# Performance work log

Hardware: AMD Instinct MI355X
Metric: run time of the kernel (lower is better)

The kernel has to match this reference:

```python
import jax, jax.numpy as jnp
import numpy as np

DEPTH, B, H, E = 4, 4096, 1024, 1024  # embedDim == h so all layers stack


def setup_inputs() -> dict:
    key = jax.random.key(0)
    k1, k2, k3, k4 = jax.random.split(key, 4)
    x = jax.random.normal(k1, (B, E), dtype=jnp.float32)
    s_h = jax.random.normal(k2, (DEPTH, B, H), dtype=jnp.float32)
    s_c = jax.random.normal(k3, (DEPTH, B, H), dtype=jnp.float32)
    # Linear(embedDim + h, 4h) per layer; stored as [in, out] (transposed torch layout)
    W = jax.random.normal(k4, (DEPTH, E + H, 4 * H), dtype=jnp.float32) * 0.02
    b = jnp.zeros((DEPTH, 4 * H), dtype=jnp.float32)
    return {"x": x, "s_h": s_h, "s_c": s_c, "W": W, "b": b}


def _lstm_layer(out, layer_params):
    hh, c, Wl, bl = layer_params
    xh = jnp.concatenate([out, hh], axis=1)          # [B, E+H]
    z = xh @ Wl + bl                                  # [B, 4H]
    i, f, o, g = jnp.split(z, 4, axis=1)              # torch.split(Wx, h, 1) order: i,f,o,g
    i = jax.nn.sigmoid(i)
    f = jax.nn.sigmoid(f)
    o = jax.nn.sigmoid(o)
    g = jnp.tanh(g)
    # trainable=False -> no dropout on g
    c_new = c * f + g * i
    h_new = jnp.tanh(c_new) * o
    return h_new, (h_new, c_new)


def reference(x, s_h, s_c, W, b):
    # scan over depth: layer l consumes previous layer's output as its input
    out, (h_new, c_new) = jax.lax.scan(_lstm_layer, x, (s_h, s_c, W, b))
    return out, h_new, c_new
```

## Files before the change

kernel.cpp:

```cpp
#include <hip/hip_runtime.h>
#include <hip/hip_bf16.h>
#include <stdint.h>

#define DEPTH 4
#define Bb 4096
#define Hh 1024
#define Ee 1024
#define Kd 2048
#define Ng 4096

typedef __attribute__((ext_vector_type(8))) short short8;
typedef __attribute__((ext_vector_type(4))) float floatx4;
typedef __attribute__((ext_vector_type(4))) float f32x4;

__device__ __forceinline__ float fast_sigmoid(float x) {
  return 1.0f / (1.0f + __expf(-x));
}
__device__ __forceinline__ float fast_tanh(float x) {
  float t = __expf(-2.0f * fabsf(x));
  return copysignf((1.0f - t) / (1.0f + t), x);
}

__device__ __forceinline__ void gload_lds16(const void* g, void* l) {
  __builtin_amdgcn_global_load_lds(
      (const __attribute__((address_space(1))) void*)(uintptr_t)g,
      (__attribute__((address_space(3))) void*)(uint32_t)(uintptr_t)l,
      16, 0, 0);
}

__global__ __launch_bounds__(256) void transpose_w_kernel(
    const float* __restrict__ W, __hip_bfloat16* __restrict__ Wt) {
  __shared__ float tile[32][33];
  const int l = blockIdx.z;
  const int n0 = blockIdx.x * 32;
  const int k0 = blockIdx.y * 32;
  const float* Wl = W + (size_t)l * Kd * Ng;
  __hip_bfloat16* Wtl = Wt + (size_t)l * Ng * Kd;
  const int tx = threadIdx.x, ty = threadIdx.y;
#pragma unroll
  for (int q = 0; q < 4; q++) {
    tile[ty + q * 8][tx] = Wl[(size_t)(k0 + ty + q * 8) * Ng + n0 + tx];
  }
  __syncthreads();
#pragma unroll
  for (int q = 0; q < 4; q++) {
    Wtl[(size_t)(n0 + ty + q * 8) * Kd + k0 + tx] =
        __float2bfloat16(tile[tx][ty + q * 8]);
  }
}

__global__ __launch_bounds__(256) void prefill_xh_kernel(
    const float* __restrict__ x, const float* __restrict__ s_h,
    __hip_bfloat16* __restrict__ xh) {
  const int idx = blockIdx.x * blockDim.x + threadIdx.x;
  const int XN = Bb * Ee / 4;
  const int TOTAL = XN + DEPTH * Bb * Hh / 4;
  if (idx >= TOTAL) return;
  const float* srcp;
  __hip_bfloat16* dst;
  if (idx < XN) {
    const int b = idx >> 8;
    const int j4 = idx & 255;
    srcp = x + (size_t)idx * 4;
    dst = xh + (size_t)b * Kd + j4 * 4;
  } else {
    const int e4 = idx - XN;
    const int l = e4 >> 20;
    const int r = e4 & 0xFFFFF;
    const int b = r >> 8;
    const int j4 = r & 255;
    srcp = s_h + (size_t)e4 * 4;
    dst = xh + (size_t)l * Bb * Kd + (size_t)b * Kd + Ee + j4 * 4;
  }
  f32x4 v = *(const f32x4*)srcp;
  union {
    __hip_bfloat16 h[4];
    unsigned long long u;
  } p;
  p.h[0] = __float2bfloat16(v.x);
  p.h[1] = __float2bfloat16(v.y);
  p.h[2] = __float2bfloat16(v.z);
  p.h[3] = __float2bfloat16(v.w);
  *(unsigned long long*)dst = p.u;
}

__global__ __launch_bounds__(256, 2) void lstm_layer_kernel(
    const __hip_bfloat16* __restrict__ A, const __hip_bfloat16* __restrict__ Wt,
    const float* __restrict__ bias, const float* __restrict__ c_in,
    float* __restrict__ out_h, float* __restrict__ out_c,
    float* __restrict__ out_final, __hip_bfloat16* __restrict__ xh_next) {
  __shared__ __attribute__((aligned(16))) __hip_bfloat16 As[128][32];
  __shared__ __attribute__((aligned(16))) __hip_bfloat16 Bs[128][32];

  const int tid = threadIdx.x;
  const int lane = tid & 63;
  const int wave = tid >> 6;
  const int wm = wave >> 1;
  const int wn = wave & 1;
  const int m0 = blockIdx.y * 128;
  const int j0 = blockIdx.x * 32;

  const int seg = (tid & 3) * 8;
  const int ra0 = tid >> 2;
  const int ra1 = (tid + 256) >> 2;
  const __hip_bfloat16* a_src0 = A + (size_t)(m0 + ra0) * Kd + seg;
  const __hip_bfloat16* a_src1 = A + (size_t)(m0 + ra1) * Kd + seg;
  const int nb0 = (ra0 >> 5) * Hh + j0 + (ra0 & 31);
  const int nb1 = (ra1 >> 5) * Hh + j0 + (ra1 & 31);
  const __hip_bfloat16* b_src0 = Wt + (size_t)nb0 * Kd + seg;
  const __hip_bfloat16* b_src1 = Wt + (size_t)nb1 * Kd + seg;
  __hip_bfloat16* a_dst0 = &As[0][0] + tid * 8;
  __hip_bfloat16* a_dst1 = &As[0][0] + (tid + 256) * 8;
  __hip_bfloat16* b_dst0 = &Bs[0][0] + tid * 8;
  __hip_bfloat16* b_dst1 = &Bs[0][0] + (tid + 256) * 8;

  floatx4 acc[4][4];
#pragma unroll
  for (int mi = 0; mi < 4; mi++)
#pragma unroll
    for (int g = 0; g < 4; g++) acc[mi][g] = floatx4{0.f, 0.f, 0.f, 0.f};

  const int lm = lane & 15;
  const int qk = lane >> 4;

  for (int kt = 0; kt < Kd / 32; kt++) {
    const int koff = kt * 32;
    __syncthreads();
    gload_lds16(a_src0 + koff, a_dst0);
    gload_lds16(a_src1 + koff, a_dst1);
    gload_lds16(b_src0 + koff, b_dst0);
    gload_lds16(b_src1 + koff, b_dst1);
    __syncthreads();

    short8 afrag[4], bfrag[4];
#pragma unroll
    for (int mi = 0; mi < 4; mi++)
      afrag[mi] = *(const short8*)&As[wm * 64 + mi * 16 + lm][qk * 8];
#pragma unroll
    for (int g = 0; g < 4; g++)
      bfrag[g] = *(const short8*)&Bs[g * 32 + wn * 16 + lm][qk * 8];
#pragma unroll
    for (int mi = 0; mi < 4; mi++)
#pragma unroll
      for (int g = 0; g < 4; g++)
        acc[mi][g] = __builtin_amdgcn_mfma_f32_16x16x32_bf16(
            afrag[mi], bfrag[g], acc[mi][g], 0, 0, 0);
  }

  const int j = j0 + wn * 16 + lm;
  const float bi = bias[j];
  const float bf = bias[Hh + j];
  const float bo = bias[2 * Hh + j];
  const float bg = bias[3 * Hh + j];
#pragma unroll
  for (int mi = 0; mi < 4; mi++) {
    const int row0 = m0 + wm * 64 + mi * 16 + qk * 4;
#pragma unroll
    for (int r = 0; r < 4; r++) {
      const int row = row0 + r;
      const float zi = acc[mi][0][r] + bi;
      const float zf = acc[mi][1][r] + bf;
      const float zo = acc[mi][2][r] + bo;
      const float zg = acc[mi][3][r] + bg;
      const float ig = fast_sigmoid(zi);
      const float fg = fast_sigmoid(zf);
      const float og = fast_sigmoid(zo);
      const float gg = fast_tanh(zg);
      const float c = c_in[(size_t)row * Hh + j];
      const float cn = fmaf(c, fg, gg * ig);
      const float hn = fast_tanh(cn) * og;
      out_h[(size_t)row * Hh + j] = hn;
      out_c[(size_t)row * Hh + j] = cn;
      if (xh_next) xh_next[(size_t)row * Kd + j] = __float2bfloat16(hn);
      if (out_final) out_final[(size_t)row * Hh + j] = hn;
    }
  }
}

extern "C" void kernel_launch(void* const* d_in, const int* in_sizes, int n_in,
                              void* d_out, int out_size, void* d_ws,
                              size_t ws_size, hipStream_t stream) {
  const float* x = (const float*)d_in[0];
  const float* s_h = (const float*)d_in[1];
  const float* s_c = (const float*)d_in[2];
  const float* W = (const float*)d_in[3];
  const float* bias = (const float*)d_in[4];
  float* out = (float*)d_out;

  __hip_bfloat16* Wt = (__hip_bfloat16*)d_ws;
  __hip_bfloat16* xh =
      (__hip_bfloat16*)((char*)d_ws + (size_t)DEPTH * Ng * Kd * 2);

  transpose_w_kernel<<<dim3(Ng / 32, Kd / 32, DEPTH), dim3(32, 8), 0, stream>>>(
      W, Wt);
  prefill_xh_kernel<<<(Bb * Ee / 4 + DEPTH * Bb * Hh / 4) / 256, 256, 0,
                      stream>>>(x, s_h, xh);

  float* out_h = out + (size_t)Bb * Ee;
  float* out_c = out_h + (size_t)DEPTH * Bb * Hh;
  for (int l = 0; l < DEPTH; l++) {
    lstm_layer_kernel<<<dim3(Hh / 32, Bb / 128), 256, 0, stream>>>(
        xh + (size_t)l * Bb * Kd, Wt + (size_t)l * Ng * Kd,
        bias + (size_t)l * Ng, s_c + (size_t)l * Bb * Hh,
        out_h + (size_t)l * Bb * Hh, out_c + (size_t)l * Bb * Hh,
        (l == DEPTH - 1) ? out : nullptr,
        (l < DEPTH - 1) ? xh + (size_t)(l + 1) * Bb * Kd : nullptr);
  }
}
```

Measured before the change: 757.7 us.

## Swizzle GEMM LDS tiles and vectorize weight transpose kernel

The GEMM's LDS tiles get an XOR swizzle on the 16-byte chunk index, applied to the global source offsets used by global_load_lds and to the fragment read offsets, to cut LDS bank conflicts on the MFMA fragment loads. Fragment offsets are precomputed once, outside the k-loop. The weight transpose kernel is rewritten to use float4 global loads into a wider padded tile and 16-byte bf16 stores of 8 k-values per thread, to improve memory coalescing. The swizzle must stay consistent between the load and read paths, and the new transpose tile has a different shared-memory bank pattern.

Measured after the change: 753.9 us. No clear change (-0.5%).

```diff
diff --git a/kernel.cpp b/kernel.cpp
--- a/kernel.cpp
+++ b/kernel.cpp
@@ -30,23 +30,30 @@
 
 __global__ __launch_bounds__(256) void transpose_w_kernel(
     const float* __restrict__ W, __hip_bfloat16* __restrict__ Wt) {
-  __shared__ float tile[32][33];
+  __shared__ __attribute__((aligned(16))) float tile[32][68];
   const int l = blockIdx.z;
-  const int n0 = blockIdx.x * 32;
-  const int k0 = blockIdx.y * 32;
-  const float* Wl = W + (size_t)l * Kd * Ng;
+  const int k0 = blockIdx.x * 32;
+  const int n0 = blockIdx.y * 64;
+  const float* Wl = W + (size_t)l * Kd * Ng + (size_t)k0 * Ng + n0;
   __hip_bfloat16* Wtl = Wt + (size_t)l * Ng * Kd;
-  const int tx = threadIdx.x, ty = threadIdx.y;
-#pragma unroll
-  for (int q = 0; q < 4; q++) {
-    tile[ty + q * 8][tx] = Wl[(size_t)(k0 + ty + q * 8) * Ng + n0 + tx];
+  const int tid = threadIdx.x;
+  {
+    const int c0 = tid, c1 = tid + 256;
+    const f32x4 v0 = *(const f32x4*)(Wl + (size_t)(c0 >> 4) * Ng + (c0 & 15) * 4);
+    const f32x4 v1 = *(const f32x4*)(Wl + (size_t)(c1 >> 4) * Ng + (c1 & 15) * 4);
+    *(f32x4*)&tile[c0 >> 4][(c0 & 15) * 4] = v0;
+    *(f32x4*)&tile[c1 >> 4][(c1 & 15) * 4] = v1;
   }
   __syncthreads();
-#pragma unroll
-  for (int q = 0; q < 4; q++) {
-    Wtl[(size_t)(n0 + ty + q * 8) * Kd + k0 + tx] =
-        __float2bfloat16(tile[tx][ty + q * 8]);
-  }
+  const int n = tid >> 2;
+  const int kc = tid & 3;
+  union {
+    __hip_bfloat16 h[8];
+    short8 s;
+  } p;
+#pragma unroll
+  for (int i = 0; i < 8; i++) p.h[i] = __float2bfloat16(tile[kc * 8 + i][n]);
+  *(short8*)&Wtl[(size_t)(n0 + n) * Kd + k0 + kc * 8] = p.s;
 }
 
 __global__ __launch_bounds__(256) void prefill_xh_kernel(
@@ -89,8 +96,8 @@
     const float* __restrict__ bias, const float* __restrict__ c_in,
     float* __restrict__ out_h, float* __restrict__ out_c,
     float* __restrict__ out_final, __hip_bfloat16* __restrict__ xh_next) {
-  __shared__ __attribute__((aligned(16))) __hip_bfloat16 As[128][32];
-  __shared__ __attribute__((aligned(16))) __hip_bfloat16 Bs[128][32];
+  __shared__ __attribute__((aligned(16))) __hip_bfloat16 As[128 * 32];
+  __shared__ __attribute__((aligned(16))) __hip_bfloat16 Bs[128 * 32];
 
   const int tid = threadIdx.x;
   const int lane = tid & 63;
@@ -100,19 +107,19 @@
   const int m0 = blockIdx.y * 128;
   const int j0 = blockIdx.x * 32;
 
-  const int seg = (tid & 3) * 8;
-  const int ra0 = tid >> 2;
-  const int ra1 = (tid + 256) >> 2;
-  const __hip_bfloat16* a_src0 = A + (size_t)(m0 + ra0) * Kd + seg;
-  const __hip_bfloat16* a_src1 = A + (size_t)(m0 + ra1) * Kd + seg;
-  const int nb0 = (ra0 >> 5) * Hh + j0 + (ra0 & 31);
-  const int nb1 = (ra1 >> 5) * Hh + j0 + (ra1 & 31);
-  const __hip_bfloat16* b_src0 = Wt + (size_t)nb0 * Kd + seg;
-  const __hip_bfloat16* b_src1 = Wt + (size_t)nb1 * Kd + seg;
-  __hip_bfloat16* a_dst0 = &As[0][0] + tid * 8;
-  __hip_bfloat16* a_dst1 = &As[0][0] + (tid + 256) * 8;
-  __hip_bfloat16* b_dst0 = &Bs[0][0] + tid * 8;
-  __hip_bfloat16* b_dst1 = &Bs[0][0] + (tid + 256) * 8;
+  const int s0 = tid, s1 = tid + 256;
+  const int r0 = s0 >> 2, q0 = (s0 & 3) ^ ((r0 >> 1) & 3);
+  const int r1 = s1 >> 2, q1 = (s1 & 3) ^ ((r1 >> 1) & 3);
+  const __hip_bfloat16* a_src0 = A + (size_t)(m0 + r0) * Kd + q0 * 8;
+  const __hip_bfloat16* a_src1 = A + (size_t)(m0 + r1) * Kd + q1 * 8;
+  const int nb0 = (r0 >> 5) * Hh + j0 + (r0 & 31);
+  const int nb1 = (r1 >> 5) * Hh + j0 + (r1 & 31);
+  const __hip_bfloat16* b_src0 = Wt + (size_t)nb0 * Kd + q0 * 8;
+  const __hip_bfloat16* b_src1 = Wt + (size_t)nb1 * Kd + q1 * 8;
+  __hip_bfloat16* a_dst0 = As + s0 * 8;
+  __hip_bfloat16* a_dst1 = As + s1 * 8;
+  __hip_bfloat16* b_dst0 = Bs + s0 * 8;
+  __hip_bfloat16* b_dst1 = Bs + s1 * 8;
 
   floatx4 acc[4][4];
 #pragma unroll
@@ -122,6 +129,18 @@
 
   const int lm = lane & 15;
   const int qk = lane >> 4;
+
+  int a_off[4], b_off[4];
+#pragma unroll
+  for (int mi = 0; mi < 4; mi++) {
+    const int R = wm * 64 + mi * 16 + lm;
+    a_off[mi] = (R * 4 + (qk ^ ((R >> 1) & 3))) * 8;
+  }
+#pragma unroll
+  for (int g = 0; g < 4; g++) {
+    const int T = g * 32 + wn * 16 + lm;
+    b_off[g] = (T * 4 + (qk ^ ((T >> 1) & 3))) * 8;
+  }
 
   for (int kt = 0; kt < Kd / 32; kt++) {
     const int koff = kt * 32;
@@ -134,11 +153,9 @@
 
     short8 afrag[4], bfrag[4];
 #pragma unroll
-    for (int mi = 0; mi < 4; mi++)
-      afrag[mi] = *(const short8*)&As[wm * 64 + mi * 16 + lm][qk * 8];
-#pragma unroll
-    for (int g = 0; g < 4; g++)
-      bfrag[g] = *(const short8*)&Bs[g * 32 + wn * 16 + lm][qk * 8];
+    for (int mi = 0; mi < 4; mi++) afrag[mi] = *(const short8*)&As[a_off[mi]];
+#pragma unroll
+    for (int g = 0; g < 4; g++) bfrag[g] = *(const short8*)&Bs[b_off[g]];
 #pragma unroll
     for (int mi = 0; mi < 4; mi++)
 #pragma unroll
@@ -191,8 +208,7 @@
   __hip_bfloat16* xh =
       (__hip_bfloat16*)((char*)d_ws + (size_t)DEPTH * Ng * Kd * 2);
 
-  transpose_w_kernel<<<dim3(Ng / 32, Kd / 32, DEPTH), dim3(32, 8), 0, stream>>>(
-      W, Wt);
+  transpose_w_kernel<<<dim3(Kd / 32, Ng / 64, DEPTH), 256, 0, stream>>>(W, Wt);
   prefill_xh_kernel<<<(Bb * Ee / 4 + DEPTH * Bb * Hh / 4) / 256, 256, 0,
                       stream>>>(x, s_h, xh);
 
```
